# Kernel tuning notes

Hardware: AMD Instinct MI355X
Metric: run time of the kernel (lower is better)

Reference implementation:

```python
import jax, jax.numpy as jnp
import numpy as np

CLASS_NUM = 2048


def full_conv(a, b):
    """Full 1D complex convolution along the last axis (no conjugation),
    identical math to convolution_new (correlation with flipped kernel ==
    standard full convolution). Computed via FFT for efficiency."""
    n = a.shape[-1] + b.shape[-1] - 1
    return jnp.fft.ifft(jnp.fft.fft(a, n) * jnp.fft.fft(b, n))


def setup_inputs() -> dict:
    key = jax.random.key(0)
    ks = jax.random.split(key, 6)
    B, N = 4096, 1024
    K0, KL = 129, 257
    return {
        "x_real": jax.random.normal(ks[0], (B, N), jnp.float32),
        "x_imag": jax.random.normal(ks[1], (B, N), jnp.float32),
        "w0_real": jax.random.normal(ks[2], (K0,), jnp.float32) / K0,
        "w0_imag": jax.random.normal(ks[3], (K0,), jnp.float32) / K0,
        "wl_real": jax.random.normal(ks[4], (KL,), jnp.float32) / KL,
        "wl_imag": jax.random.normal(ks[5], (KL,), jnp.float32) / KL,
    }


def reference(x_real, x_imag, w0_real, w0_imag, wl_real, wl_imag):
    x = (x_real + 1j * x_imag).astype(jnp.complex64)      # [B, 1024]
    w0 = (w0_real + 1j * w0_imag).astype(jnp.complex64)   # [129]
    wl = (wl_real + 1j * wl_imag).astype(jnp.complex64)   # [257]

    # ConvList stage 0: full conv with weight_0 (expand=True broadcasts 1D weight)
    h = full_conv(x, w0)          # [B, 1152]
    # ConvSelfLayer_new: full autoconvolution of h with itself
    h = full_conv(h, h)           # [B, 2303]
    # Last conv with weightLast
    y = full_conv(h, wl)          # [B, 2559]

    # center-crop to classNum, then magnitude
    offset = (y.shape[-1] - CLASS_NUM) // 2  # == 255; matches module's parity rule
    return jnp.abs(y[:, offset:offset + CLASS_NUM])  # [B, 2048] float32
```

## Files before the change

### kernel.cpp

```cpp
#include <hip/hip_runtime.h>
#include <math.h>

#define NFFT 4096
#define T    256
#define ROWS 4096
#define NX   1024
#define OUTN 2048
#define OFF  255

__device__ __forceinline__ float2 cmulf(float2 a, float2 b) {
  return make_float2(a.x * b.x - a.y * b.y, a.x * b.y + a.y * b.x);
}
__device__ __forceinline__ float2 caddf(float2 a, float2 b) {
  return make_float2(a.x + b.x, a.y + b.y);
}
__device__ __forceinline__ float2 csubf(float2 a, float2 b) {
  return make_float2(a.x - b.x, a.y - b.y);
}
template <int DIR> __device__ __forceinline__ float2 mulmi(float2 a) {
  return (DIR > 0) ? make_float2(a.y, -a.x) : make_float2(-a.y, a.x);
}
template <int DIR> __device__ __forceinline__ float2 cmulc(float2 a, float wr, float wi) {
  const float y = (DIR > 0) ? wi : -wi;
  return make_float2(a.x * wr - a.y * y, a.x * y + a.y * wr);
}

#define C16 0.9238795325112867f
#define S16 0.3826834323650898f
#define RH  0.7071067811865476f

template <int DIR>
__device__ __forceinline__ void dft16(const float2* v, float2* o) {
  float2 f[16];
#pragma unroll
  for (int r = 0; r < 4; ++r) {
    const float2 a = v[r], b = v[r + 4], c = v[r + 8], d = v[r + 12];
    const float2 apc = caddf(a, c), amc = csubf(a, c);
    const float2 bpd = caddf(b, d), bmd = csubf(b, d);
    const float2 jb = mulmi<DIR>(bmd);
    f[r]      = caddf(apc, bpd);
    f[r + 4]  = caddf(amc, jb);
    f[r + 8]  = csubf(apc, bpd);
    f[r + 12] = csubf(amc, jb);
  }
  f[5]  = cmulc<DIR>(f[5],  C16, -S16);
  f[6]  = cmulc<DIR>(f[6],  RH,  -RH);
  f[7]  = cmulc<DIR>(f[7],  S16, -C16);
  f[9]  = cmulc<DIR>(f[9],  RH,  -RH);
  f[10] = mulmi<DIR>(f[10]);
  f[11] = cmulc<DIR>(f[11], -RH, -RH);
  f[13] = cmulc<DIR>(f[13], S16, -C16);
  f[14] = cmulc<DIR>(f[14], -RH, -RH);
  f[15] = cmulc<DIR>(f[15], -C16, S16);
#pragma unroll
  for (int c4 = 0; c4 < 4; ++c4) {
    const float2 a = f[4 * c4], b = f[4 * c4 + 1], c = f[4 * c4 + 2], d = f[4 * c4 + 3];
    const float2 apc = caddf(a, c), amc = csubf(a, c);
    const float2 bpd = caddf(b, d), bmd = csubf(b, d);
    const float2 jb = mulmi<DIR>(bmd);
    o[c4]      = caddf(apc, bpd);
    o[c4 + 4]  = caddf(amc, jb);
    o[c4 + 8]  = csubf(apc, bpd);
    o[c4 + 12] = csubf(amc, jb);
  }
}

template <int DIR>
__device__ __forceinline__ void dft16_sp4(const float2* v, float2* o) {
#pragma unroll
  for (int c4 = 0; c4 < 4; ++c4) {
    const float2 a = v[0];
    const float2 b = (c4 == 0) ? v[1]
                   : (c4 == 1) ? cmulc<DIR>(v[1], C16, -S16)
                   : (c4 == 2) ? cmulc<DIR>(v[1], RH, -RH)
                               : cmulc<DIR>(v[1], S16, -C16);
    const float2 c = (c4 == 0) ? v[2]
                   : (c4 == 1) ? cmulc<DIR>(v[2], RH, -RH)
                   : (c4 == 2) ? mulmi<DIR>(v[2])
                               : cmulc<DIR>(v[2], -RH, -RH);
    const float2 d = (c4 == 0) ? v[3]
                   : (c4 == 1) ? cmulc<DIR>(v[3], S16, -C16)
                   : (c4 == 2) ? cmulc<DIR>(v[3], -RH, -RH)
                               : cmulc<DIR>(v[3], -C16, S16);
    const float2 apc = caddf(a, c), amc = csubf(a, c);
    const float2 bpd = caddf(b, d), bmd = csubf(b, d);
    const float2 jb = mulmi<DIR>(bmd);
    o[c4]      = caddf(apc, bpd);
    o[c4 + 4]  = caddf(amc, jb);
    o[c4 + 8]  = csubf(apc, bpd);
    o[c4 + 12] = csubf(amc, jb);
  }
}

__device__ __forceinline__ void chain_apply(float2* u, float2 step) {
  float2 w = step;
  u[1] = cmulf(u[1], w);
#pragma unroll
  for (int c = 2; c < 16; ++c) { w = cmulf(w, step); u[c] = cmulf(u[c], w); }
}
__device__ __forceinline__ void chain_apply_base(float2* u, float2 base, float2 step) {
  float2 w = base;
  u[0] = cmulf(u[0], w);
#pragma unroll
  for (int c = 1; c < 16; ++c) { w = cmulf(w, step); u[c] = cmulf(u[c], w); }
}

__global__ __launch_bounds__(256) void init_tables(
    const float* __restrict__ w0r, const float* __restrict__ w0i,
    const float* __restrict__ wlr, const float* __restrict__ wli,
    float2* __restrict__ G, float2* __restrict__ tw) {
  const int f = blockIdx.x * blockDim.x + threadIdx.x;
  if (f >= NFFT) return;
  const float cconst = -2.0f * 3.14159265358979323846f / (float)NFFT;
  float w0re = 0.f, w0im = 0.f;
  for (int n = 0; n < 129; ++n) {
    const int mfn = (f * n) & (NFFT - 1);
    float sv, cv;
    __sincosf(cconst * (float)mfn, &sv, &cv);
    const float ar = w0r[n], ai = w0i[n];
    w0re += ar * cv - ai * sv;
    w0im += ar * sv + ai * cv;
  }
  float wlre = 0.f, wlim = 0.f;
  for (int n = 0; n < 257; ++n) {
    const int mfn = (f * n) & (NFFT - 1);
    float sv, cv;
    __sincosf(cconst * (float)mfn, &sv, &cv);
    const float ar = wlr[n], ai = wli[n];
    wlre += ar * cv - ai * sv;
    wlim += ar * sv + ai * cv;
  }
  const float2 W0 = make_float2(w0re, w0im);
  const float2 WL = make_float2(wlre, wlim);
  const float2 g = cmulf(cmulf(W0, W0), WL);
  G[f] = make_float2(g.x * (1.0f / NFFT), g.y * (1.0f / NFFT));
  float sv, cv;
  __sincosf(cconst * (float)f, &sv, &cv);
  tw[f] = make_float2(cv, sv);
}

__global__ __launch_bounds__(T, 4) void conv_fft(
    const float* __restrict__ xr, const float* __restrict__ xi,
    const float2* __restrict__ G, const float2* __restrict__ tw,
    float* __restrict__ out) {
  __shared__ float2 L[16 * 257];
  const int row = blockIdx.x;
  const int t = threadIdx.x;
  const int n1 = t & 15;
  const int hi = t >> 4;
  const float* __restrict__ rr = xr + (size_t)row * NX;
  const float* __restrict__ ri = xi + (size_t)row * NX;

  float2 e[16], u[16];
#pragma unroll
  for (int m = 0; m < 4; ++m) e[m] = make_float2(rr[t + 256 * m], ri[t + 256 * m]);

  dft16_sp4<1>(e, u);
  { float2 s1 = tw[16 * hi]; chain_apply(u, s1); }
#pragma unroll
  for (int c = 0; c < 16; ++c) L[c * 256 + t] = u[c];
  __syncthreads();
#pragma unroll
  for (int m1 = 0; m1 < 16; ++m1) e[m1] = L[hi * 256 + m1 * 16 + n1];
  __syncthreads();
  dft16<1>(e, u);
  { float2 b2 = tw[n1 * hi]; float2 s2 = tw[16 * n1]; chain_apply_base(u, b2, s2); }
#pragma unroll
  for (int j1 = 0; j1 < 16; ++j1) L[n1 * 257 + hi + 16 * j1] = u[j1];
  __syncthreads();
#pragma unroll
  for (int q = 0; q < 16; ++q) e[q] = L[q * 257 + t];
  dft16<1>(e, u);

#pragma unroll
  for (int k = 0; k < 16; ++k) {
    const float2 X = u[k];
    e[k] = cmulf(cmulf(X, X), G[t + 256 * k]);
  }
  __syncthreads();

  dft16<-1>(e, u);
  { float2 s1 = tw[16 * hi]; s1.y = -s1.y; chain_apply(u, s1); }
#pragma unroll
  for (int c = 0; c < 16; ++c) L[c * 256 + t] = u[c];
  __syncthreads();
#pragma unroll
  for (int m1 = 0; m1 < 16; ++m1) e[m1] = L[hi * 256 + m1 * 16 + n1];
  __syncthreads();
  dft16<-1>(e, u);
  { float2 b2 = tw[n1 * hi]; b2.y = -b2.y;
    float2 s2 = tw[16 * n1]; s2.y = -s2.y; chain_apply_base(u, b2, s2); }
#pragma unroll
  for (int j1 = 0; j1 < 16; ++j1) L[n1 * 257 + hi + 16 * j1] = u[j1];
  __syncthreads();
#pragma unroll
  for (int q = 0; q < 16; ++q) e[q] = L[q * 257 + t];
  dft16<-1>(e, u);

  float* __restrict__ orow = out + (size_t)row * OUTN;
#pragma unroll
  for (int k = 1; k < 8; ++k) {
    const float2 y = u[k];
    orow[t + 256 * k - OFF] = sqrtf(y.x * y.x + y.y * y.y);
  }
  if (t == 255) { const float2 y = u[0]; orow[0] = sqrtf(y.x * y.x + y.y * y.y); }
  if (t < 255)  { const float2 y = u[8]; orow[1793 + t] = sqrtf(y.x * y.x + y.y * y.y); }
}

extern "C" void kernel_launch(void* const* d_in, const int* in_sizes, int n_in,
                              void* d_out, int out_size, void* d_ws, size_t ws_size,
                              hipStream_t stream) {
  const float* xr  = (const float*)d_in[0];
  const float* xi  = (const float*)d_in[1];
  const float* w0r = (const float*)d_in[2];
  const float* w0i = (const float*)d_in[3];
  const float* wlr = (const float*)d_in[4];
  const float* wli = (const float*)d_in[5];
  float* out = (float*)d_out;
  float2* G  = (float2*)d_ws;
  float2* tw = (float2*)((char*)d_ws + NFFT * sizeof(float2));
  hipLaunchKernelGGL(init_tables, dim3(16), dim3(256), 0, stream,
                     w0r, w0i, wlr, wli, G, tw);
  hipLaunchKernelGGL(conv_fft, dim3(ROWS), dim3(T), 0, stream,
                     xr, xi, G, tw, out);
}
```

Before: 144.6 us.

## Load twiddles from table, XOR-swizzle LDS transpose, raise occupancy bound

Replaces the recursive twiddle chains (a serial dependent multiply chain) with direct lookups into the global twiddle table for each element. The padded shared-memory layout is replaced by an unpadded 16x256 buffer with an XOR swizzle to avoid bank conflicts. The launch bound is raised to 5 waves per SIMD. The aims are shorter dependency chains and more resident blocks, at the cost of many more scattered global (cached) twiddle loads and possible register pressure.

```diff
diff --git a/kernel.cpp b/kernel.cpp
--- a/kernel.cpp
+++ b/kernel.cpp
@@ -16,6 +16,10 @@
 }
 __device__ __forceinline__ float2 csubf(float2 a, float2 b) {
   return make_float2(a.x - b.x, a.y - b.y);
+}
+template <int DIR> __device__ __forceinline__ float2 tmul(float2 a, float2 w) {
+  return (DIR > 0) ? make_float2(a.x * w.x - a.y * w.y, a.x * w.y + a.y * w.x)
+                   : make_float2(a.x * w.x + a.y * w.y, a.y * w.x - a.x * w.y);
 }
 template <int DIR> __device__ __forceinline__ float2 mulmi(float2 a) {
   return (DIR > 0) ? make_float2(a.y, -a.x) : make_float2(-a.y, a.x);
@@ -92,19 +96,6 @@
   }
 }
 
-__device__ __forceinline__ void chain_apply(float2* u, float2 step) {
-  float2 w = step;
-  u[1] = cmulf(u[1], w);
-#pragma unroll
-  for (int c = 2; c < 16; ++c) { w = cmulf(w, step); u[c] = cmulf(u[c], w); }
-}
-__device__ __forceinline__ void chain_apply_base(float2* u, float2 base, float2 step) {
-  float2 w = base;
-  u[0] = cmulf(u[0], w);
-#pragma unroll
-  for (int c = 1; c < 16; ++c) { w = cmulf(w, step); u[c] = cmulf(u[c], w); }
-}
-
 __global__ __launch_bounds__(256) void init_tables(
     const float* __restrict__ w0r, const float* __restrict__ w0i,
     const float* __restrict__ wlr, const float* __restrict__ wli,
@@ -139,11 +130,11 @@
   tw[f] = make_float2(cv, sv);
 }
 
-__global__ __launch_bounds__(T, 4) void conv_fft(
+__global__ __launch_bounds__(T, 5) void conv_fft(
     const float* __restrict__ xr, const float* __restrict__ xi,
     const float2* __restrict__ G, const float2* __restrict__ tw,
     float* __restrict__ out) {
-  __shared__ float2 L[16 * 257];
+  __shared__ float2 L[16 * 256];
   const int row = blockIdx.x;
   const int t = threadIdx.x;
   const int n1 = t & 15;
@@ -156,7 +147,8 @@
   for (int m = 0; m < 4; ++m) e[m] = make_float2(rr[t + 256 * m], ri[t + 256 * m]);
 
   dft16_sp4<1>(e, u);
-  { float2 s1 = tw[16 * hi]; chain_apply(u, s1); }
+#pragma unroll
+  for (int c = 1; c < 16; ++c) u[c] = tmul<1>(u[c], tw[16 * hi * c]);
 #pragma unroll
   for (int c = 0; c < 16; ++c) L[c * 256 + t] = u[c];
   __syncthreads();
@@ -164,12 +156,14 @@
   for (int m1 = 0; m1 < 16; ++m1) e[m1] = L[hi * 256 + m1 * 16 + n1];
   __syncthreads();
   dft16<1>(e, u);
-  { float2 b2 = tw[n1 * hi]; float2 s2 = tw[16 * n1]; chain_apply_base(u, b2, s2); }
-#pragma unroll
-  for (int j1 = 0; j1 < 16; ++j1) L[n1 * 257 + hi + 16 * j1] = u[j1];
-  __syncthreads();
-#pragma unroll
-  for (int q = 0; q < 16; ++q) e[q] = L[q * 257 + t];
+#pragma unroll
+  for (int c = 0; c < 16; ++c) u[c] = tmul<1>(u[c], tw[n1 * (hi + 16 * c)]);
+#pragma unroll
+  for (int j1 = 0; j1 < 16; ++j1)
+    L[n1 * 256 + ((hi ^ n1) + 16 * j1)] = u[j1];
+  __syncthreads();
+#pragma unroll
+  for (int q = 0; q < 16; ++q) e[q] = L[q * 256 + (t ^ q)];
   dft16<1>(e, u);
 
 #pragma unroll
@@ -180,7 +174,8 @@
   __syncthreads();
 
   dft16<-1>(e, u);
-  { float2 s1 = tw[16 * hi]; s1.y = -s1.y; chain_apply(u, s1); }
+#pragma unroll
+  for (int c = 1; c < 16; ++c) u[c] = tmul<-1>(u[c], tw[16 * hi * c]);
 #pragma unroll
   for (int c = 0; c < 16; ++c) L[c * 256 + t] = u[c];
   __syncthreads();
@@ -188,13 +183,14 @@
   for (int m1 = 0; m1 < 16; ++m1) e[m1] = L[hi * 256 + m1 * 16 + n1];
   __syncthreads();
   dft16<-1>(e, u);
-  { float2 b2 = tw[n1 * hi]; b2.y = -b2.y;
-    float2 s2 = tw[16 * n1]; s2.y = -s2.y; chain_apply_base(u, b2, s2); }
-#pragma unroll
-  for (int j1 = 0; j1 < 16; ++j1) L[n1 * 257 + hi + 16 * j1] = u[j1];
-  __syncthreads();
-#pragma unroll
-  for (int q = 0; q < 16; ++q) e[q] = L[q * 257 + t];
+#pragma unroll
+  for (int c = 0; c < 16; ++c) u[c] = tmul<-1>(u[c], tw[n1 * (hi + 16 * c)]);
+#pragma unroll
+  for (int j1 = 0; j1 < 16; ++j1)
+    L[n1 * 256 + ((hi ^ n1) + 16 * j1)] = u[j1];
+  __syncthreads();
+#pragma unroll
+  for (int q = 0; q < 16; ++q) e[q] = L[q * 256 + (t ^ q)];
   dft16<-1>(e, u);
 
   float* __restrict__ orow = out + (size_t)row * OUTN;
```

After: 309.5 us. 2.14x slower.
